# Kernel optimization log

Measured on AMD Instinct MI355X. Metric: run time of the kernel, lower is better.

The kernel has to match this reference:

```python
import math
import jax, jax.numpy as jnp
import numpy as np

COLORS = 10
MAX_SHIFT = 5
B, H, W = 32, 128, 128

_shifts = [(dy, dx) for dy in range(-MAX_SHIFT, MAX_SHIFT + 1)
           for dx in range(-MAX_SHIFT, MAX_SHIFT + 1)
           if not (dy == 0 and dx == 0)]  # include_identity=False
DYS = jnp.asarray(np.array([s[0] for s in _shifts], dtype=np.int32))
DXS = jnp.asarray(np.array([s[1] for s in _shifts], dtype=np.int32))


def _shift_all(grid):
    """Apply every (dy,dx) shift to an int grid [B,H,W] with zero padding.

    out[s, b, y, x] = grid[b, y-dy_s, x-dx_s] if in-bounds else 0,
    exactly matching apply_shift_batch (uncovered regions are color 0).
    Returns [S, B, H, W].
    """
    b, h, w = grid.shape
    padded = jnp.pad(grid, ((0, 0), (MAX_SHIFT, MAX_SHIFT), (MAX_SHIFT, MAX_SHIFT)))
    def one(dy, dx):
        return jax.lax.dynamic_slice(padded, (0, MAX_SHIFT - dy, MAX_SHIFT - dx), (b, h, w))
    return jax.vmap(one)(DYS, DXS)


def setup_inputs() -> dict:
    key = jax.random.key(0)
    k1, k2, k3 = jax.random.split(key, 3)
    return {
        "demo_in": jax.random.randint(k1, (B, H, W), 0, COLORS, dtype=jnp.int32),
        "demo_out": jax.random.randint(k2, (B, H, W), 0, COLORS, dtype=jnp.int32),
        "query_in": jax.random.randint(k3, (B, H, W), 0, COLORS, dtype=jnp.int32),
        "color_log_weight": jnp.zeros((COLORS,), dtype=jnp.float32),
        "logit_scale": jnp.asarray(4.0, dtype=jnp.float32),
    }


def reference(demo_in, demo_out, query_in, color_log_weight, logit_scale):
    b, h, w = query_in.shape
    S = DYS.shape[0]

    # Per-shift correlation score. one_hot(shifted)*one_hot(demo_out)*w summed
    # over (C,H,W) == sum over pixels of w[demo_out] * (shifted == demo_out).
    shifted_demo = _shift_all(demo_in)                       # [S,B,H,W] int
    w_out = jnp.exp(color_log_weight)[demo_out]              # [B,H,W]
    eq = (shifted_demo == demo_out[None]).astype(jnp.float32)
    match = jnp.sum(eq * w_out[None], axis=(2, 3))           # [S,B]
    scale = jnp.minimum(jnp.exp(logit_scale), 100.0)
    scores = match.T / math.sqrt(h * w) * scale              # [B,S]
    attention = jax.nn.softmax(scores, axis=1)               # [B,S]

    # Weighted accumulation of one-hot shifted queries, done as a scatter-add
    # into the color channel (avoids materializing [S,B,C,H,W]).
    shifted_query = _shift_all(query_in)                     # [S,B,H,W] int
    b_idx = jnp.arange(b)[None, :, None, None]
    y_idx = jnp.arange(h)[None, None, :, None]
    x_idx = jnp.arange(w)[None, None, None, :]
    attn_b = jnp.broadcast_to(attention.T[:, :, None, None], (S, b, h, w))
    accum = jnp.zeros((b, COLORS, h, w), dtype=jnp.float32)
    accum = accum.at[b_idx, shifted_query, y_idx, x_idx].add(attn_b)
    return jnp.log(jnp.maximum(accum, 1e-6))
```

## Files before the change

### kernel.cpp

```cpp
#include <hip/hip_runtime.h>
#include <hip/hip_bf16.h>
#include <math.h>

#define COLORS 10
#define NB 32
#define H 128
#define W 128
#define NS 120
#define HW (H*W)
#define STRIPS 8
#define SH 16
#define DROWS 26
#define DINW 12
#define AR 18

typedef unsigned char u8;
typedef unsigned int u32;
typedef unsigned long long u64;
typedef float f32x4 __attribute__((ext_vector_type(4)));
typedef short bf16x8 __attribute__((ext_vector_type(8)));

__global__ __launch_bounds__(512) void match_strip(
    const int* __restrict__ demo_in, const int* __restrict__ demo_out,
    const float* __restrict__ clw, float* __restrict__ mpart)
{
    __shared__ __align__(16) u32 din_p[COLORS][DROWS][DINW];
    __shared__ __align__(16) u32 dout_p[COLORS][SH][4];
    __shared__ float wexp[COLORS];

    int t = threadIdx.x;
    int strip = blockIdx.x;
    int b = blockIdx.y;
    int wave = t >> 6, lane = t & 63;
    int y0 = strip * SH;

    if (t < COLORS) wexp[t] = __expf(clw[t]);

    const int* di = demo_in  + b * HW;
    const int* dd = demo_out + b * HW;

    int vv0[4], vv1[4];
    bool okk[4];
    #pragma unroll
    for (int i = 0; i < 4; i++) {
        int r = wave + i * 8;
        int gy = y0 - 5 + r;
        bool ok = (r < DROWS) && (gy >= 0 && gy < H);
        int cy = (gy < 0) ? 0 : (gy > 127 ? 127 : gy);
        vv0[i] = di[cy * W + lane];
        vv1[i] = di[cy * W + 64 + lane];
        okk[i] = ok;
    }
    int w0[2], w1[2];
    #pragma unroll
    for (int i = 0; i < 2; i++) {
        int r = wave + i * 8;
        int gy = y0 + r;
        w0[i] = dd[gy * W + lane];
        w1[i] = dd[gy * W + 64 + lane];
    }

    #pragma unroll
    for (int i = 0; i < 4; i++) {
        int r = wave + i * 8;
        if (r < DROWS) {
            bool ok = okk[i];
            int v0 = ok ? vv0[i] : 0;
            int v1 = ok ? vv1[i] : 0;
            #pragma unroll
            for (int c = 0; c < COLORS; c++) {
                u64 h0 = __ballot(v0 == c);
                u64 h1 = __ballot(v1 == c);
                u64 P0, P1, P2;
                if (!ok) {
                    P0 = (c == 0) ? ~0ull : 0ull;
                    P1 = P0;
                    P2 = (c == 0) ? 0x3FFull : 0ull;
                } else {
                    u64 lm = (c == 0) ? 0x1Full  : 0ull;
                    u64 rm = (c == 0) ? 0x3E0ull : 0ull;
                    P0 = (h0 << 5) | lm;
                    P1 = (h0 >> 59) | (h1 << 5);
                    P2 = (h1 >> 59) | rm;
                }
                if (lane == 0) {
                    *reinterpret_cast<uint4*>(&din_p[c][r][0]) =
                        make_uint4((u32)P0, (u32)(P0 >> 32), (u32)P1, (u32)(P1 >> 32));
                    *reinterpret_cast<uint4*>(&din_p[c][r][4]) =
                        make_uint4((u32)P2, 0u, 0u, 0u);
                }
            }
        }
    }
    #pragma unroll
    for (int i = 0; i < 2; i++) {
        int r = wave + i * 8;
        int v0 = w0[i], v1 = w1[i];
        #pragma unroll
        for (int c = 0; c < COLORS; c++) {
            u64 h0 = __ballot(v0 == c);
            u64 h1 = __ballot(v1 == c);
            if (lane == 0)
                *reinterpret_cast<uint4*>(&dout_p[c][r][0]) =
                    make_uint4((u32)h0, (u32)(h0 >> 32), (u32)h1, (u32)(h1 >> 32));
        }
    }
    __syncthreads();

    int s = t >> 2, qq = t & 3;
    float acc = 0.f;
    if (t < 4 * NS) {
        int lin = s + (s >= 60);
        int dy = lin / 11 - 5, dx = lin % 11 - 5;
        int k = 5 - dx;
        for (int c = 0; c < COLORS; c++) {
            int cnt = 0;
            #pragma unroll
            for (int yy = 0; yy < 4; yy++) {
                int y = qq * 4 + yy;
                int r = y - dy + 5;
                const u32* dr   = &din_p[c][r][0];
                const u32* orow = &dout_p[c][y][0];
                u32 s0 = __builtin_amdgcn_alignbit(dr[1], dr[0], k);
                u32 s1 = __builtin_amdgcn_alignbit(dr[2], dr[1], k);
                u32 s2 = __builtin_amdgcn_alignbit(dr[3], dr[2], k);
                u32 s3 = __builtin_amdgcn_alignbit(dr[4], dr[3], k);
                cnt += __popc(s0 & orow[0]) + __popc(s1 & orow[1])
                     + __popc(s2 & orow[2]) + __popc(s3 & orow[3]);
            }
            acc += wexp[c] * (float)cnt;
        }
    }
    acc += __shfl_down(acc, 1, 64);
    acc += __shfl_down(acc, 2, 64);
    if (qq == 0 && t < 4 * NS)
        mpart[(b * NS + s) * STRIPS + strip] = acc;
}

__global__ __launch_bounds__(512) void accum_fused(
    const int* __restrict__ query_in, const float* __restrict__ mpart,
    const float* __restrict__ logit_scale, float* __restrict__ out)
{
    __shared__ u8  qs[AR][144];
    __shared__ float sm[NS];
    __shared__ unsigned short abf[128];
    __shared__ __align__(16) u32 Agl[11][64][4];

    int t  = threadIdx.x;
    int y0 = blockIdx.x * 8;
    int b  = blockIdx.y;
    const int* q = query_in + b * HW;

    u32 pk0 = 0, pk1 = 0;
    {
        int g = t;
        #pragma unroll
        for (int e = 0; e < 4; e++) {
            int idx = g * 4 + e;
            int r = idx / 144, p = idx - r * 144;
            int gy = y0 - 5 + r;
            bool ok = (gy >= 0) & (gy < H) & (p >= 5) & (p < 133);
            int cy = gy < 0 ? 0 : (gy > 127 ? 127 : gy);
            int cx = p < 5 ? 0 : (p > 132 ? 127 : p - 5);
            int v = q[cy * W + cx];
            pk0 |= (u32)(ok ? v : 0) << (8 * e);
        }
    }
    if (t < 648 - 512) {
        int g = t + 512;
        #pragma unroll
        for (int e = 0; e < 4; e++) {
            int idx = g * 4 + e;
            int r = idx / 144, p = idx - r * 144;
            int gy = y0 - 5 + r;
            bool ok = (gy >= 0) & (gy < H) & (p >= 5) & (p < 133);
            int cy = gy < 0 ? 0 : (gy > 127 ? 127 : gy);
            int cx = p < 5 ? 0 : (p > 132 ? 127 : p - 5);
            int v = q[cy * W + cx];
            pk1 |= (u32)(ok ? v : 0) << (8 * e);
        }
    }

    float scale = fminf(__expf(logit_scale[0]), 100.0f) * (1.0f / 128.0f);
    if (t < NS) {
        const float* mp = mpart + (t + b * NS) * STRIPS;
        float4 v0 = *reinterpret_cast<const float4*>(mp);
        float4 v1 = *reinterpret_cast<const float4*>(mp + 4);
        sm[t] = (v0.x + v0.y + v0.z + v0.w + v1.x + v1.y + v1.z + v1.w) * scale;
    }

    ((u32*)qs)[t] = pk0;
    if (t < 648 - 512) ((u32*)qs)[t + 512] = pk1;
    __syncthreads();

    if (t < 64) {
        float s0 = sm[t];
        float s1 = (t + 64 < NS) ? sm[t + 64] : -INFINITY;
        float m = fmaxf(s0, s1);
        for (int off = 32; off > 0; off >>= 1) m = fmaxf(m, __shfl_xor(m, off, 64));
        float e0 = __expf(s0 - m);
        float e1 = (t + 64 < NS) ? __expf(s1 - m) : 0.f;
        float sum = e0 + e1;
        for (int off = 32; off > 0; off >>= 1) sum += __shfl_xor(sum, off, 64);
        float inv = 1.0f / sum;
        sm[t] = e0 * inv;
        if (t + 64 < NS) sm[t + 64] = e1 * inv;
    }
    __syncthreads();
    if (t < 128) {
        unsigned short v = 0;
        if (t < 121 && t != 60) {
            int si = t - (t > 60);
            __hip_bfloat16 hb = __float2bfloat16(sm[si]);
            v = *reinterpret_cast<unsigned short*>(&hb);
        }
        abf[t] = v;
    }
    __syncthreads();

    {
        int e = t;
        int st = e >> 6, l = e & 63;
        int mrow = l & 15, g8 = (l >> 4) * 8;
        #pragma unroll
        for (int p = 0; p < 4; p++) {
            int j0 = mrow + 10 - (g8 + p * 2);
            int j1 = j0 - 1;
            int i0 = (j0 >= 0 && j0 <= 10) ? (10 - st) * 11 + j0 : 121;
            int i1 = (j1 >= 0 && j1 <= 10) ? (10 - st) * 11 + j1 : 121;
            Agl[st][l][p] = (u32)abf[i0] | ((u32)abf[i1] << 16);
        }
    }
    if (t < 704 - 512) {
        int e = t + 512;
        int st = e >> 6, l = e & 63;
        int mrow = l & 15, g8 = (l >> 4) * 8;
        #pragma unroll
        for (int p = 0; p < 4; p++) {
            int j0 = mrow + 10 - (g8 + p * 2);
            int j1 = j0 - 1;
            int i0 = (j0 >= 0 && j0 <= 10) ? (10 - st) * 11 + j0 : 121;
            int i1 = (j1 >= 0 && j1 <= 10) ? (10 - st) * 11 + j1 : 121;
            Agl[st][l][p] = (u32)abf[i0] | ((u32)abf[i1] << 16);
        }
    }
    __syncthreads();

    int lane = t & 63, w = t >> 6;
    int x0 = w * 16;
    int c = lane & 15, g = lane >> 4;

    #define BUILD_B(r) ({                                                        \
        u64 eight = *reinterpret_cast<const u64*>(&qs[(r)][x0 + 8 * g]);         \
        u32 lo = (u32)eight, hi = (u32)(eight >> 32);                            \
        u32 b0 = ((int)(lo & 255) == c ? 0x3F80u : 0u)                           \
               | ((int)((lo >> 8)  & 255) == c ? 0x3F800000u : 0u);              \
        u32 b1 = ((int)((lo >> 16) & 255) == c ? 0x3F80u : 0u)                   \
               | ((int)((lo >> 24) & 255) == c ? 0x3F800000u : 0u);              \
        u32 b2 = ((int)(hi & 255) == c ? 0x3F80u : 0u)                           \
               | ((int)((hi >> 8)  & 255) == c ? 0x3F800000u : 0u);              \
        u32 b3 = ((int)((hi >> 16) & 255) == c ? 0x3F80u : 0u)                   \
               | ((int)((hi >> 24) & 255) == c ? 0x3F800000u : 0u);              \
        make_uint4(b0, b1, b2, b3); })

    uint4 bf[8];
    #pragma unroll
    for (int r = 0; r < 7; r++) bf[r & 7] = BUILD_B(r);

    f32x4 acc0[4], acc1[4];
    #pragma unroll
    for (int j = 0; j < 4; j++) { acc0[j] = (f32x4){0,0,0,0}; acc1[j] = (f32x4){0,0,0,0}; }

    #pragma unroll
    for (int st = 0; st < 11; st++) {
        bf[(st + 7) & 7] = BUILD_B(st + 7);
        uint4 a4 = *reinterpret_cast<const uint4*>(&Agl[st][lane][0]);
        union { uint4 u; bf16x8 v; } A; A.u = a4;
        #pragma unroll
        for (int j = 0; j < 4; j++) {
            union { uint4 u; bf16x8 v; } B0, B1;
            B0.u = bf[(st + j) & 7];
            B1.u = bf[(st + 4 + j) & 7];
            acc0[j] = __builtin_amdgcn_mfma_f32_16x16x32_bf16(A.v, B0.v, acc0[j], 0, 0, 0);
            acc1[j] = __builtin_amdgcn_mfma_f32_16x16x32_bf16(A.v, B1.v, acc1[j], 0, 0, 0);
        }
    }
    #undef BUILD_B

    if (c < COLORS) {
        #pragma unroll
        for (int j = 0; j < 4; j++) {
            float* ob0 = out + (((size_t)b * COLORS + c) * H + (y0 + j)) * W + x0 + 4 * g;
            float4 r0;
            r0.x = __logf(fmaxf(acc0[j][0], 1e-6f));
            r0.y = __logf(fmaxf(acc0[j][1], 1e-6f));
            r0.z = __logf(fmaxf(acc0[j][2], 1e-6f));
            r0.w = __logf(fmaxf(acc0[j][3], 1e-6f));
            *reinterpret_cast<float4*>(ob0) = r0;
            float* ob1 = out + (((size_t)b * COLORS + c) * H + (y0 + 4 + j)) * W + x0 + 4 * g;
            float4 r1;
            r1.x = __logf(fmaxf(acc1[j][0], 1e-6f));
            r1.y = __logf(fmaxf(acc1[j][1], 1e-6f));
            r1.z = __logf(fmaxf(acc1[j][2], 1e-6f));
            r1.w = __logf(fmaxf(acc1[j][3], 1e-6f));
            *reinterpret_cast<float4*>(ob1) = r1;
        }
    }
}

__global__ __launch_bounds__(256) void match_kernel(
    const int* __restrict__ demo_in, const int* __restrict__ demo_out,
    const float* __restrict__ clw, float* __restrict__ match)
{
    int blk = blockIdx.x;
    int b = blk / NS;
    int s = blk % NS;
    int lin = s + (s >= 60 ? 1 : 0);
    int dy = lin / 11 - 5, dx = lin % 11 - 5;

    __shared__ float wexp[COLORS];
    int tid = threadIdx.x;
    if (tid < COLORS) wexp[tid] = expf(clw[tid]);
    __syncthreads();

    const int* __restrict__ din  = demo_in  + b * HW;
    const int* __restrict__ dout = demo_out + b * HW;

    float partial = 0.f;
    for (int i = tid; i < HW; i += 256) {
        int yy = i >> 7, xx = i & 127;
        int co = dout[i];
        int sy = yy - dy, sx = xx - dx;
        int v = 0;
        if (sy >= 0 && sy < H && sx >= 0 && sx < W) v = din[sy * W + sx];
        if (v == co) partial += wexp[co];
    }
    for (int off = 32; off > 0; off >>= 1) partial += __shfl_down(partial, off, 64);
    __shared__ float wsum[4];
    if ((tid & 63) == 0) wsum[tid >> 6] = partial;
    __syncthreads();
    if (tid == 0) match[blk] = wsum[0] + wsum[1] + wsum[2] + wsum[3];
}

__global__ __launch_bounds__(64) void softmax_kernel(
    const float* __restrict__ match, const float* __restrict__ logit_scale,
    float* __restrict__ attention)
{
    int b = blockIdx.x;
    int lane = threadIdx.x;
    float scale = fminf(expf(logit_scale[0]), 100.0f) / sqrtf((float)HW);
    int i0 = lane, i1 = lane + 64;
    float s0 = match[b * NS + i0] * scale;
    float s1 = (i1 < NS) ? match[b * NS + i1] * scale : -INFINITY;
    float m = fmaxf(s0, s1);
    for (int off = 32; off > 0; off >>= 1) m = fmaxf(m, __shfl_xor(m, off, 64));
    float e0 = expf(s0 - m);
    float e1 = (i1 < NS) ? expf(s1 - m) : 0.f;
    float sum = e0 + e1;
    for (int off = 32; off > 0; off >>= 1) sum += __shfl_xor(sum, off, 64);
    float inv = 1.0f / sum;
    attention[b * NS + i0] = e0 * inv;
    if (i1 < NS) attention[b * NS + i1] = e1 * inv;
}

__global__ __launch_bounds__(128) void accum_kernel(
    const int* __restrict__ query_in, const float* __restrict__ attention,
    float* __restrict__ out)
{
    int blk = blockIdx.x;
    int b = blk >> 7;
    int y = blk & 127;
    int x = threadIdx.x;

    __shared__ float att[NS];
    if (threadIdx.x < NS) att[threadIdx.x] = attention[b * NS + threadIdx.x];
    __syncthreads();

    const int* __restrict__ q = query_in + b * HW;
    float acc[COLORS];
    #pragma unroll
    for (int c = 0; c < COLORS; c++) acc[c] = 0.f;

    #pragma unroll 4
    for (int s = 0; s < NS; s++) {
        int lin = s + (s >= 60 ? 1 : 0);
        int dy = lin / 11 - 5, dx = lin % 11 - 5;
        int sy = y - dy, sx = x - dx;
        int v = 0;
        if (sy >= 0 && sy < H && sx >= 0 && sx < W) v = q[sy * W + sx];
        float a = att[s];
        #pragma unroll
        for (int c = 0; c < COLORS; c++) acc[c] += (v == c) ? a : 0.f;
    }
    float* __restrict__ ob = out + (size_t)b * COLORS * HW + y * W + x;
    #pragma unroll
    for (int c = 0; c < COLORS; c++) ob[c * HW] = __logf(fmaxf(acc[c], 1e-6f));
}

extern "C" void kernel_launch(void* const* d_in, const int* in_sizes, int n_in,
                              void* d_out, int out_size, void* d_ws, size_t ws_size,
                              hipStream_t stream) {
    const int*   demo_in     = (const int*)d_in[0];
    const int*   demo_out    = (const int*)d_in[1];
    const int*   query_in    = (const int*)d_in[2];
    const float* clw         = (const float*)d_in[3];
    const float* logit_scale = (const float*)d_in[4];
    float* out = (float*)d_out;

    size_t needed = (size_t)NB * NS * STRIPS * sizeof(float);

    if (ws_size >= needed) {
        float* mpart = (float*)d_ws;
        match_strip<<<dim3(STRIPS, NB), 512, 0, stream>>>(demo_in, demo_out, clw, mpart);
        accum_fused<<<dim3(H / 8, NB), 512, 0, stream>>>(query_in, mpart, logit_scale, out);
    } else {
        float* match = (float*)d_ws;
        float* att   = match + NB * NS;
        match_kernel<<<NB * NS, 256, 0, stream>>>(demo_in, demo_out, clw, match);
        softmax_kernel<<<NB, 64, 0, stream>>>(match, logit_scale, att);
        accum_kernel<<<NB * H, 128, 0, stream>>>(query_in, att, out);
    }
}
```

Before: 28.35 us.

## Split softmax and A-fragment build into separate kernel, halve accum tile height

Moves the softmax and the bf16 A-matrix construction out of the accumulation kernel into a small per-batch kernel that writes A fragments to workspace. The accumulation kernel then processes 4 rows per block instead of 8, doubling the grid, and loads A fragments directly into registers. This removes the softmax and A-build work that every accumulation block repeated, and is meant to raise occupancy. In exchange it adds a third kernel launch, a global round-trip for the A fragments, and a larger halo overhead per output row.

```diff
diff --git a/kernel.cpp b/kernel.cpp
--- a/kernel.cpp
+++ b/kernel.cpp
@@ -137,49 +137,14 @@
         mpart[(b * NS + s) * STRIPS + strip] = acc;
 }
 
-__global__ __launch_bounds__(512) void accum_fused(
-    const int* __restrict__ query_in, const float* __restrict__ mpart,
-    const float* __restrict__ logit_scale, float* __restrict__ out)
-{
-    __shared__ u8  qs[AR][144];
+__global__ __launch_bounds__(128) void softmax_abuild(
+    const float* __restrict__ mpart, const float* __restrict__ logit_scale,
+    uint4* __restrict__ Agl_g)
+{
     __shared__ float sm[NS];
     __shared__ unsigned short abf[128];
-    __shared__ __align__(16) u32 Agl[11][64][4];
-
-    int t  = threadIdx.x;
-    int y0 = blockIdx.x * 8;
-    int b  = blockIdx.y;
-    const int* q = query_in + b * HW;
-
-    u32 pk0 = 0, pk1 = 0;
-    {
-        int g = t;
-        #pragma unroll
-        for (int e = 0; e < 4; e++) {
-            int idx = g * 4 + e;
-            int r = idx / 144, p = idx - r * 144;
-            int gy = y0 - 5 + r;
-            bool ok = (gy >= 0) & (gy < H) & (p >= 5) & (p < 133);
-            int cy = gy < 0 ? 0 : (gy > 127 ? 127 : gy);
-            int cx = p < 5 ? 0 : (p > 132 ? 127 : p - 5);
-            int v = q[cy * W + cx];
-            pk0 |= (u32)(ok ? v : 0) << (8 * e);
-        }
-    }
-    if (t < 648 - 512) {
-        int g = t + 512;
-        #pragma unroll
-        for (int e = 0; e < 4; e++) {
-            int idx = g * 4 + e;
-            int r = idx / 144, p = idx - r * 144;
-            int gy = y0 - 5 + r;
-            bool ok = (gy >= 0) & (gy < H) & (p >= 5) & (p < 133);
-            int cy = gy < 0 ? 0 : (gy > 127 ? 127 : gy);
-            int cx = p < 5 ? 0 : (p > 132 ? 127 : p - 5);
-            int v = q[cy * W + cx];
-            pk1 |= (u32)(ok ? v : 0) << (8 * e);
-        }
-    }
+    int b = blockIdx.x;
+    int t = threadIdx.x;
 
     float scale = fminf(__expf(logit_scale[0]), 100.0f) * (1.0f / 128.0f);
     if (t < NS) {
@@ -188,11 +153,7 @@
         float4 v1 = *reinterpret_cast<const float4*>(mp + 4);
         sm[t] = (v0.x + v0.y + v0.z + v0.w + v1.x + v1.y + v1.z + v1.w) * scale;
     }
-
-    ((u32*)qs)[t] = pk0;
-    if (t < 648 - 512) ((u32*)qs)[t + 512] = pk1;
-    __syncthreads();
-
+    __syncthreads();
     if (t < 64) {
         float s0 = sm[t];
         float s1 = (t + 64 < NS) ? sm[t + 64] : -INFINITY;
@@ -218,35 +179,60 @@
     }
     __syncthreads();
 
-    {
-        int e = t;
-        int st = e >> 6, l = e & 63;
-        int mrow = l & 15, g8 = (l >> 4) * 8;
-        #pragma unroll
-        for (int p = 0; p < 4; p++) {
-            int j0 = mrow + 10 - (g8 + p * 2);
-            int j1 = j0 - 1;
-            int i0 = (j0 >= 0 && j0 <= 10) ? (10 - st) * 11 + j0 : 121;
-            int i1 = (j1 >= 0 && j1 <= 10) ? (10 - st) * 11 + j1 : 121;
-            Agl[st][l][p] = (u32)abf[i0] | ((u32)abf[i1] << 16);
-        }
-    }
-    if (t < 704 - 512) {
-        int e = t + 512;
-        int st = e >> 6, l = e & 63;
-        int mrow = l & 15, g8 = (l >> 4) * 8;
-        #pragma unroll
-        for (int p = 0; p < 4; p++) {
-            int j0 = mrow + 10 - (g8 + p * 2);
-            int j1 = j0 - 1;
-            int i0 = (j0 >= 0 && j0 <= 10) ? (10 - st) * 11 + j0 : 121;
-            int i1 = (j1 >= 0 && j1 <= 10) ? (10 - st) * 11 + j1 : 121;
-            Agl[st][l][p] = (u32)abf[i0] | ((u32)abf[i1] << 16);
-        }
-    }
-    __syncthreads();
-
+    #pragma unroll
+    for (int base = 0; base < 768; base += 128) {
+        int e = t + base;
+        if (e < 704) {
+            int st = e >> 6, l = e & 63;
+            int mrow = l & 15, g8 = (l >> 4) * 8;
+            u32 wq[4];
+            #pragma unroll
+            for (int p = 0; p < 4; p++) {
+                int j0 = mrow + 10 - (g8 + p * 2);
+                int j1 = j0 - 1;
+                int i0 = (j0 >= 0 && j0 <= 10) ? (10 - st) * 11 + j0 : 121;
+                int i1 = (j1 >= 0 && j1 <= 10) ? (10 - st) * 11 + j1 : 121;
+                wq[p] = (u32)abf[i0] | ((u32)abf[i1] << 16);
+            }
+            Agl_g[((size_t)b * 11 + st) * 64 + l] = make_uint4(wq[0], wq[1], wq[2], wq[3]);
+        }
+    }
+}
+
+__global__ __launch_bounds__(512, 4) void accum_mfma4(
+    const int* __restrict__ query_in, const uint4* __restrict__ Agl_g,
+    float* __restrict__ out)
+{
+    __shared__ u8 qs[14][144];
+    int t  = threadIdx.x;
+    int y0 = blockIdx.x * 4;
+    int b  = blockIdx.y;
+    const int* q = query_in + b * HW;
     int lane = t & 63, w = t >> 6;
+
+    u32 pk0 = 0;
+    if (t < 504) {
+        #pragma unroll
+        for (int e = 0; e < 4; e++) {
+            int idx = t * 4 + e;
+            int r = idx / 144, p = idx - r * 144;
+            int gy = y0 - 5 + r;
+            bool ok = (gy >= 0) & (gy < H) & (p >= 5) & (p < 133);
+            int cy = gy < 0 ? 0 : (gy > 127 ? 127 : gy);
+            int cx = p < 5 ? 0 : (p > 132 ? 127 : p - 5);
+            int v = q[cy * W + cx];
+            pk0 |= (u32)(ok ? v : 0) << (8 * e);
+        }
+    }
+
+    uint4 afr[11];
+    #pragma unroll
+    for (int st = 0; st < 11; st++)
+        afr[st] = Agl_g[((size_t)b * 11 + st) * 64 + lane];
+
+    if (t < 504) ((u32*)qs)[t] = pk0;
+    __syncthreads();
+
     int x0 = w * 16;
     int c = lane & 15, g = lane >> 4;
 
@@ -267,15 +253,174 @@
     #pragma unroll
     for (int r = 0; r < 7; r++) bf[r & 7] = BUILD_B(r);
 
+    f32x4 acc[4];
+    #pragma unroll
+    for (int j = 0; j < 4; j++) acc[j] = (f32x4){0.f, 0.f, 0.f, 0.f};
+
+    #pragma unroll
+    for (int st = 0; st < 11; st++) {
+        if (st < 7) bf[(st + 7) & 7] = BUILD_B(st + 7);
+        union { uint4 u; bf16x8 v; } A; A.u = afr[st];
+        #pragma unroll
+        for (int j = 0; j < 4; j++) {
+            union { uint4 u; bf16x8 v; } B; B.u = bf[(st + j) & 7];
+            acc[j] = __builtin_amdgcn_mfma_f32_16x16x32_bf16(A.v, B.v, acc[j], 0, 0, 0);
+        }
+    }
+    #undef BUILD_B
+
+    if (c < COLORS) {
+        #pragma unroll
+        for (int j = 0; j < 4; j++) {
+            float* ob = out + (((size_t)b * COLORS + c) * H + (y0 + j)) * W + x0 + 4 * g;
+            float4 rr;
+            rr.x = __logf(fmaxf(acc[j][0], 1e-6f));
+            rr.y = __logf(fmaxf(acc[j][1], 1e-6f));
+            rr.z = __logf(fmaxf(acc[j][2], 1e-6f));
+            rr.w = __logf(fmaxf(acc[j][3], 1e-6f));
+            *reinterpret_cast<float4*>(ob) = rr;
+        }
+    }
+}
+
+__global__ __launch_bounds__(512) void accum_fused(
+    const int* __restrict__ query_in, const float* __restrict__ mpart,
+    const float* __restrict__ logit_scale, float* __restrict__ out)
+{
+    __shared__ u8  qs[AR][144];
+    __shared__ float sm[NS];
+    __shared__ unsigned short abf[128];
+    __shared__ __align__(16) u32 Agl[11][64][4];
+
+    int t  = threadIdx.x;
+    int y0 = blockIdx.x * 8;
+    int b  = blockIdx.y;
+    const int* q = query_in + b * HW;
+
+    u32 pk0 = 0, pk1 = 0;
+    {
+        int g = t;
+        #pragma unroll
+        for (int e = 0; e < 4; e++) {
+            int idx = g * 4 + e;
+            int r = idx / 144, p = idx - r * 144;
+            int gy = y0 - 5 + r;
+            bool ok = (gy >= 0) & (gy < H) & (p >= 5) & (p < 133);
+            int cy = gy < 0 ? 0 : (gy > 127 ? 127 : gy);
+            int cx = p < 5 ? 0 : (p > 132 ? 127 : p - 5);
+            int v = q[cy * W + cx];
+            pk0 |= (u32)(ok ? v : 0) << (8 * e);
+        }
+    }
+    if (t < 648 - 512) {
+        int g = t + 512;
+        #pragma unroll
+        for (int e = 0; e < 4; e++) {
+            int idx = g * 4 + e;
+            int r = idx / 144, p = idx - r * 144;
+            int gy = y0 - 5 + r;
+            bool ok = (gy >= 0) & (gy < H) & (p >= 5) & (p < 133);
+            int cy = gy < 0 ? 0 : (gy > 127 ? 127 : gy);
+            int cx = p < 5 ? 0 : (p > 132 ? 127 : p - 5);
+            int v = q[cy * W + cx];
+            pk1 |= (u32)(ok ? v : 0) << (8 * e);
+        }
+    }
+
+    float scale = fminf(__expf(logit_scale[0]), 100.0f) * (1.0f / 128.0f);
+    if (t < NS) {
+        const float* mp = mpart + (t + b * NS) * STRIPS;
+        float4 v0 = *reinterpret_cast<const float4*>(mp);
+        float4 v1 = *reinterpret_cast<const float4*>(mp + 4);
+        sm[t] = (v0.x + v0.y + v0.z + v0.w + v1.x + v1.y + v1.z + v1.w) * scale;
+    }
+
+    ((u32*)qs)[t] = pk0;
+    if (t < 648 - 512) ((u32*)qs)[t + 512] = pk1;
+    __syncthreads();
+
+    if (t < 64) {
+        float s0 = sm[t];
+        float s1 = (t + 64 < NS) ? sm[t + 64] : -INFINITY;
+        float m = fmaxf(s0, s1);
+        for (int off = 32; off > 0; off >>= 1) m = fmaxf(m, __shfl_xor(m, off, 64));
+        float e0 = __expf(s0 - m);
+        float e1 = (t + 64 < NS) ? __expf(s1 - m) : 0.f;
+        float sum = e0 + e1;
+        for (int off = 32; off > 0; off >>= 1) sum += __shfl_xor(sum, off, 64);
+        float inv = 1.0f / sum;
+        sm[t] = e0 * inv;
+        if (t + 64 < NS) sm[t + 64] = e1 * inv;
+    }
+    __syncthreads();
+    if (t < 128) {
+        unsigned short v = 0;
+        if (t < 121 && t != 60) {
+            int si = t - (t > 60);
+            __hip_bfloat16 hb = __float2bfloat16(sm[si]);
+            v = *reinterpret_cast<unsigned short*>(&hb);
+        }
+        abf[t] = v;
+    }
+    __syncthreads();
+
+    {
+        int e = t;
+        int st = e >> 6, l = e & 63;
+        int mrow = l & 15, g8 = (l >> 4) * 8;
+        #pragma unroll
+        for (int p = 0; p < 4; p++) {
+            int j0 = mrow + 10 - (g8 + p * 2);
+            int j1 = j0 - 1;
+            int i0 = (j0 >= 0 && j0 <= 10) ? (10 - st) * 11 + j0 : 121;
+            int i1 = (j1 >= 0 && j1 <= 10) ? (10 - st) * 11 + j1 : 121;
+            Agl[st][l][p] = (u32)abf[i0] | ((u32)abf[i1] << 16);
+        }
+    }
+    if (t < 704 - 512) {
+        int e = t + 512;
+        int st = e >> 6, l = e & 63;
+        int mrow = l & 15, g8 = (l >> 4) * 8;
+        #pragma unroll
+        for (int p = 0; p < 4; p++) {
+            int j0 = mrow + 10 - (g8 + p * 2);
+            int j1 = j0 - 1;
+            int i0 = (j0 >= 0 && j0 <= 10) ? (10 - st) * 11 + j0 : 121;
+            int i1 = (j1 >= 0 && j1 <= 10) ? (10 - st) * 11 + j1 : 121;
+            Agl[st][l][p] = (u32)abf[i0] | ((u32)abf[i1] << 16);
+        }
+    }
+    __syncthreads();
+
+    int lane = t & 63, w = t >> 6;
+    int x0 = w * 16;
+    int c = lane & 15, g = lane >> 4;
+
+    #define BUILD_B2(r) ({                                                       \
+        u64 eight = *reinterpret_cast<const u64*>(&qs[(r)][x0 + 8 * g]);         \
+        u32 lo = (u32)eight, hi = (u32)(eight >> 32);                            \
+        u32 b0 = ((int)(lo & 255) == c ? 0x3F80u : 0u)                           \
+               | ((int)((lo >> 8)  & 255) == c ? 0x3F800000u : 0u);              \
+        u32 b1 = ((int)((lo >> 16) & 255) == c ? 0x3F80u : 0u)                   \
+               | ((int)((lo >> 24) & 255) == c ? 0x3F800000u : 0u);              \
+        u32 b2 = ((int)(hi & 255) == c ? 0x3F80u : 0u)                           \
+               | ((int)((hi >> 8)  & 255) == c ? 0x3F800000u : 0u);              \
+        u32 b3 = ((int)((hi >> 16) & 255) == c ? 0x3F80u : 0u)                   \
+               | ((int)((hi >> 24) & 255) == c ? 0x3F800000u : 0u);              \
+        make_uint4(b0, b1, b2, b3); })
+
+    uint4 bf[8];
+    #pragma unroll
+    for (int r = 0; r < 7; r++) bf[r & 7] = BUILD_B2(r);
+
     f32x4 acc0[4], acc1[4];
     #pragma unroll
     for (int j = 0; j < 4; j++) { acc0[j] = (f32x4){0,0,0,0}; acc1[j] = (f32x4){0,0,0,0}; }
 
     #pragma unroll
     for (int st = 0; st < 11; st++) {
-        bf[(st + 7) & 7] = BUILD_B(st + 7);
-        uint4 a4 = *reinterpret_cast<const uint4*>(&Agl[st][lane][0]);
-        union { uint4 u; bf16x8 v; } A; A.u = a4;
+        bf[(st + 7) & 7] = BUILD_B2(st + 7);
+        union { uint4 u; bf16x8 v; } A; A.u = *reinterpret_cast<const uint4*>(&Agl[st][lane][0]);
         #pragma unroll
         for (int j = 0; j < 4; j++) {
             union { uint4 u; bf16x8 v; } B0, B1;
@@ -285,7 +430,7 @@
             acc1[j] = __builtin_amdgcn_mfma_f32_16x16x32_bf16(A.v, B1.v, acc1[j], 0, 0, 0);
         }
     }
-    #undef BUILD_B
+    #undef BUILD_B2
 
     if (c < COLORS) {
         #pragma unroll
@@ -407,9 +552,17 @@
     const float* logit_scale = (const float*)d_in[4];
     float* out = (float*)d_out;
 
-    size_t needed = (size_t)NB * NS * STRIPS * sizeof(float);
-
-    if (ws_size >= needed) {
+    size_t mpart_sz = (size_t)NB * NS * STRIPS * sizeof(float);
+    size_t agl_sz   = (size_t)NB * 11 * 64 * sizeof(uint4);
+    size_t need3    = mpart_sz + agl_sz;
+
+    if (ws_size >= need3) {
+        float* mpart = (float*)d_ws;
+        uint4* Agl_g = (uint4*)((char*)d_ws + mpart_sz);
+        match_strip<<<dim3(STRIPS, NB), 512, 0, stream>>>(demo_in, demo_out, clw, mpart);
+        softmax_abuild<<<NB, 128, 0, stream>>>(mpart, logit_scale, Agl_g);
+        accum_mfma4<<<dim3(H / 4, NB), 512, 0, stream>>>(query_in, Agl_g, out);
+    } else if (ws_size >= mpart_sz) {
         float* mpart = (float*)d_ws;
         match_strip<<<dim3(STRIPS, NB), 512, 0, stream>>>(demo_in, demo_out, clw, mpart);
         accum_fused<<<dim3(H / 8, NB), 512, 0, stream>>>(query_in, mpart, logit_scale, out);
```

Result: slower. 31.81 us (+12.2%).
